# Kernel tuning notes

Measured on AMD Instinct MI355X. Metric: run time of the kernel, lower is better.

The kernel has to match this reference:

```python
import jax, jax.numpy as jnp
import numpy as np

N_GRAPHS = 128


def setup_inputs() -> dict:
    key = jax.random.key(0)
    k1, k2, k3, k4, k5, k6, k7 = jax.random.split(key, 7)
    N, E, IN, HID, OUT = 50000, 800000, 64, 64, 2
    x = jax.random.normal(k1, (N, IN), dtype=jnp.float32)
    edge_index = jax.random.randint(k2, (2, E), 0, N, dtype=jnp.int64)
    batch = jnp.sort(jax.random.randint(k3, (N,), 0, N_GRAPHS, dtype=jnp.int64))
    # GCNConv params (glorot-ish) and output Linear params
    W = jax.random.normal(k4, (IN, HID), dtype=jnp.float32) / np.sqrt(IN)
    b = jnp.zeros((HID,), dtype=jnp.float32)
    lin_W = jax.random.normal(k5, (HID, OUT), dtype=jnp.float32) / np.sqrt(HID)
    lin_b = jax.random.normal(k6, (OUT,), dtype=jnp.float32) * 0.01
    return {"x": x, "edge_index": edge_index, "batch": batch,
            "W": W, "b": b, "lin_W": lin_W, "lin_b": lin_b}


def gcn_conv(x, edge_index, W, b):
    N = x.shape[0]
    # add self loops (PyG GCNConv default)
    loop = jnp.arange(N, dtype=edge_index.dtype)
    row = jnp.concatenate([edge_index[0], loop])  # source nodes
    col = jnp.concatenate([edge_index[1], loop])  # target nodes
    # symmetric degree normalization D^{-1/2} (A+I) D^{-1/2}
    deg = jax.ops.segment_sum(jnp.ones_like(col, dtype=x.dtype), col, num_segments=N)
    dinv = jnp.where(deg > 0, jax.lax.rsqrt(jnp.maximum(deg, 1e-12)), 0.0)
    norm = dinv[row] * dinv[col]  # [E+N]
    h = x @ W  # [N, HID] transform before aggregation
    msgs = norm[:, None] * h[row]  # [E+N, HID] gathered messages
    out = jax.ops.segment_sum(msgs, col, num_segments=N)
    return out + b


def reference(x, edge_index, batch, W, b, lin_W, lin_b):
    h = gcn_conv(x, edge_index, W, b)
    h = jax.nn.relu(h)
    # global mean pool over batch ids
    sums = jax.ops.segment_sum(h, batch, num_segments=N_GRAPHS)  # [G, HID]
    cnts = jax.ops.segment_sum(jnp.ones((h.shape[0],), h.dtype), batch, num_segments=N_GRAPHS)
    pooled = sums / jnp.maximum(cnts, 1.0)[:, None]
    # dropout(p=0.2) is identity in eval mode
    return pooled @ lin_W + lin_b  # [G, OUT]
```

## Files before the change

kernel.cpp:

```cpp
#include <hip/hip_runtime.h>
#include <hip/hip_fp16.h>

#define N_NODES 50000
#define N_EDGES 800000
#define FDIM    64
#define NGRAPH  128
#define CAP     64
#define GW      8
#define NPB     32
#define NGSLOT  8
#define NBLK1   200
#define CHUNK_E (N_EDGES / NBLK1)
#define CHUNK_I4 (CHUNK_E / 4)
#define NBKT    196
#define SEGC    64


__global__ void k_bin(const int4* __restrict__ row4, const int4* __restrict__ col4,
                      unsigned int* __restrict__ gbin, int* __restrict__ gcnt,
                      float* __restrict__ pooled, float* __restrict__ cnt) {
    __shared__ unsigned int sbuf[NBKT * SEGC];
    __shared__ int scnt[NBKT];
    int tid = threadIdx.x, blk = blockIdx.x;
    if (blk == 0) {
        float4 z = make_float4(0.f, 0.f, 0.f, 0.f);
        float4* p4 = (float4*)pooled;
        for (int i = tid; i < (NGRAPH * FDIM) / 4; i += 256) p4[i] = z;
        float4* c4 = (float4*)cnt;
        if (tid < NGRAPH / 4) c4[tid] = z;
    }
    for (int i = tid; i < NBKT; i += 256) scnt[i] = 0;
    __syncthreads();
    int base = blk * CHUNK_I4;
    for (int i = base + tid; i < base + CHUNK_I4; i += 256) {
        int4 c = col4[i];
        int4 r = row4[i];
        int s, p;
        s = c.x >> 8; p = atomicAdd(&scnt[s], 1);
        if (p < SEGC) sbuf[s * SEGC + p] = ((unsigned)(c.x & 255) << 16) | (unsigned)r.x;
        s = c.y >> 8; p = atomicAdd(&scnt[s], 1);
        if (p < SEGC) sbuf[s * SEGC + p] = ((unsigned)(c.y & 255) << 16) | (unsigned)r.y;
        s = c.z >> 8; p = atomicAdd(&scnt[s], 1);
        if (p < SEGC) sbuf[s * SEGC + p] = ((unsigned)(c.z & 255) << 16) | (unsigned)r.z;
        s = c.w >> 8; p = atomicAdd(&scnt[s], 1);
        if (p < SEGC) sbuf[s * SEGC + p] = ((unsigned)(c.w & 255) << 16) | (unsigned)r.w;
    }
    __syncthreads();
    const uint4* s4 = (const uint4*)sbuf;
    uint4* g4 = (uint4*)(gbin + (size_t)blk * (NBKT * SEGC));
    for (int i = tid; i < NBKT * SEGC / 4; i += 256) g4[i] = s4[i];
    for (int s = tid; s < NBKT; s += 256) gcnt[s * NBLK1 + blk] = min(scnt[s], SEGC);
}

__global__ void k_commit(const unsigned int* __restrict__ gbin, const int* __restrict__ gcnt,
                         int* __restrict__ fill, unsigned short* __restrict__ ew) {
    __shared__ int cnts[NBLK1];
    __shared__ int fl[256];
    __shared__ unsigned short slots[256 * CAP];
    int b = blockIdx.x, tid = threadIdx.x;
    for (int i = tid; i < NBLK1; i += 256) cnts[i] = gcnt[b * NBLK1 + i];
    fl[tid] = 0;
    __syncthreads();
    for (int idx = tid; idx < NBLK1 * SEGC; idx += 256) {
        int seg = idx >> 6, j = idx & 63;
        if (j < cnts[seg]) {
            unsigned int v = gbin[((size_t)seg * NBKT + b) * SEGC + j];
            int cl = (int)(v >> 16);
            int p = atomicAdd(&fl[cl], 1);
            if (p < CAP) slots[(cl << 6) + p] = (unsigned short)(v & 0xffffu);
        }
    }
    __syncthreads();
    int nd0 = b << 8;
    int nnodes = min(256, N_NODES - nd0);
    uint4* e4 = (uint4*)(ew + ((size_t)nd0 << 6));
    const uint4* s4 = (const uint4*)slots;
    for (int i = tid; i < nnodes * 8; i += 256) e4[i] = s4[i];
    if (tid < nnodes) fill[nd0 + tid] = fl[tid];
}

__global__ void k_gemm_xw(const float* __restrict__ x, const float* __restrict__ W,
                          const int* __restrict__ fill, __half* __restrict__ h2, int n) {
    int f = threadIdx.x & 63;
    int w = threadIdx.x >> 6;
    float Wreg[FDIM];
    #pragma unroll
    for (int k = 0; k < FDIM; ++k) Wreg[k] = W[k * FDIM + f];
    for (int nd = blockIdx.x * 4 + w; nd < n; nd += gridDim.x * 4) {
        const float4* xr4 = (const float4*)(x + (size_t)nd * FDIM);
        float acc = 0.0f;
        #pragma unroll
        for (int k4 = 0; k4 < 16; ++k4) {
            float4 xv = xr4[k4];
            acc = fmaf(xv.x, Wreg[4 * k4],     acc);
            acc = fmaf(xv.y, Wreg[4 * k4 + 1], acc);
            acc = fmaf(xv.z, Wreg[4 * k4 + 2], acc);
            acc = fmaf(xv.w, Wreg[4 * k4 + 3], acc);
        }
        float di = rsqrtf((float)(fill[nd] + 1));
        h2[((size_t)nd << 6) + f] = __float2half(di * acc);
    }
}

#define ACC4(U, AX, AY, AZ, AW)                                        \
    {                                                                  \
        float2 lo_ = __half22float2(*(const __half2*)&(U).x);          \
        float2 hi_ = __half22float2(*(const __half2*)&(U).y);          \
        AX += lo_.x; AY += lo_.y; AZ += hi_.x; AW += hi_.y;            \
    }

__global__ void k_gather_pool(const int* __restrict__ fill, const unsigned short* __restrict__ ew,
                              const uint2* __restrict__ h2q, const float* __restrict__ b,
                              const int* __restrict__ batch,
                              float* __restrict__ pooled, float* __restrict__ cnt) {
    __shared__ float pl[NGSLOT][FDIM];
    __shared__ float pcnt[NGSLOT];
    __shared__ int g_first_s;

    int tid = threadIdx.x;
    int lane    = tid & 63;
    int fp      = lane & 15;
    int quarter = lane >> 4;
    int wv  = tid >> 6;
    int blk0 = blockIdx.x * NPB;

    for (int i = tid; i < NGSLOT * FDIM; i += 256) pl[i >> 6][i & 63] = 0.0f;
    if (tid < NGSLOT) pcnt[tid] = 0.0f;
    if (tid == 0) g_first_s = batch[blk0];
    __syncthreads();
    int g_first = g_first_s;

    int start = blk0 + wv * GW;
    bool active = start < N_NODES;

    if (active) {
        int dg8 = fill[start + (lane & 7)];
        int bt8 = batch[start + (lane & 7)];
        int slots = (int)ew[((size_t)start << 6) + lane];

        float b0 = b[4 * fp], b1 = b[4 * fp + 1], b2 = b[4 * fp + 2], b3 = b[4 * fp + 3];
        float p0 = 0, p1 = 0, p2 = 0, p3 = 0, cacc = 0;
        int gcur = __shfl(bt8, 0);
        #pragma unroll
        for (int i = 0; i < GW; ++i) {
            int nd = start + i;
            int slots_next = (i < GW - 1) ? (int)ew[((size_t)(nd + 1) << 6) + lane] : 0;
            int g = __shfl(bt8, i);
            if (g != gcur) {
                int sl = gcur - g_first;
                if (sl >= 0 && sl < NGSLOT) {
                    if (quarter == 0) {
                        atomicAdd(&pl[sl][4 * fp],     p0);
                        atomicAdd(&pl[sl][4 * fp + 1], p1);
                        atomicAdd(&pl[sl][4 * fp + 2], p2);
                        atomicAdd(&pl[sl][4 * fp + 3], p3);
                    }
                    if (lane == 0) atomicAdd(&pcnt[sl], cacc);
                } else {
                    if (quarter == 0) {
                        atomicAdd(&pooled[gcur * FDIM + 4 * fp],     p0);
                        atomicAdd(&pooled[gcur * FDIM + 4 * fp + 1], p1);
                        atomicAdd(&pooled[gcur * FDIM + 4 * fp + 2], p2);
                        atomicAdd(&pooled[gcur * FDIM + 4 * fp + 3], p3);
                    }
                    if (lane == 0) atomicAdd(&cnt[gcur], cacc);
                }
                p0 = p1 = p2 = p3 = 0; cacc = 0; gcur = g;
            }
            int deg = min(__shfl(dg8, i), CAP);
            float a0x = 0, a0y = 0, a0z = 0, a0w = 0;
            float a1x = 0, a1y = 0, a1z = 0, a1w = 0;
            float a2x = 0, a2y = 0, a2z = 0, a2w = 0;
            float a3x = 0, a3y = 0, a3z = 0, a3w = 0;
            if (quarter == 0) {
                uint2 su = h2q[((size_t)nd << 4) + fp];
                ACC4(su, a0x, a0y, a0z, a0w);
            }
            int e = 0;
            for (; e + 16 <= deg; e += 16) {
                int s0 = __shfl(slots, e + quarter);
                int s1 = __shfl(slots, e + 4 + quarter);
                int s2 = __shfl(slots, e + 8 + quarter);
                int s3 = __shfl(slots, e + 12 + quarter);
                uint2 u0 = h2q[((size_t)s0 << 4) + fp];
                uint2 u1 = h2q[((size_t)s1 << 4) + fp];
                uint2 u2 = h2q[((size_t)s2 << 4) + fp];
                uint2 u3 = h2q[((size_t)s3 << 4) + fp];
                ACC4(u0, a0x, a0y, a0z, a0w);
                ACC4(u1, a1x, a1y, a1z, a1w);
                ACC4(u2, a2x, a2y, a2z, a2w);
                ACC4(u3, a3x, a3y, a3z, a3w);
            }
            for (; e < deg; e += 4) {
                int idx = e + quarter;
                int sx = __shfl(slots, idx < deg ? idx : deg - 1);
                uint2 u = h2q[((size_t)sx << 4) + fp];
                if (idx < deg) ACC4(u, a0x, a0y, a0z, a0w);
            }
            float ax = (a0x + a1x) + (a2x + a3x);
            float ay = (a0y + a1y) + (a2y + a3y);
            float az = (a0z + a1z) + (a2z + a3z);
            float aw = (a0w + a1w) + (a2w + a3w);
            ax += __shfl_xor(ax, 16); ax += __shfl_xor(ax, 32);
            ay += __shfl_xor(ay, 16); ay += __shfl_xor(ay, 32);
            az += __shfl_xor(az, 16); az += __shfl_xor(az, 32);
            aw += __shfl_xor(aw, 16); aw += __shfl_xor(aw, 32);
            float di = rsqrtf((float)(deg + 1));
            p0 += fmaxf(fmaf(di, ax, b0), 0.0f);
            p1 += fmaxf(fmaf(di, ay, b1), 0.0f);
            p2 += fmaxf(fmaf(di, az, b2), 0.0f);
            p3 += fmaxf(fmaf(di, aw, b3), 0.0f);
            cacc += 1.0f;
            slots = slots_next;
        }
        {
            int sl = gcur - g_first;
            if (sl >= 0 && sl < NGSLOT) {
                if (quarter == 0) {
                    atomicAdd(&pl[sl][4 * fp],     p0);
                    atomicAdd(&pl[sl][4 * fp + 1], p1);
                    atomicAdd(&pl[sl][4 * fp + 2], p2);
                    atomicAdd(&pl[sl][4 * fp + 3], p3);
                }
                if (lane == 0) atomicAdd(&pcnt[sl], cacc);
            } else {
                if (quarter == 0) {
                    atomicAdd(&pooled[gcur * FDIM + 4 * fp],     p0);
                    atomicAdd(&pooled[gcur * FDIM + 4 * fp + 1], p1);
                    atomicAdd(&pooled[gcur * FDIM + 4 * fp + 2], p2);
                    atomicAdd(&pooled[gcur * FDIM + 4 * fp + 3], p3);
                }
                if (lane == 0) atomicAdd(&cnt[gcur], cacc);
            }
        }
    }
    __syncthreads();
    for (int idx = tid; idx < NGSLOT * FDIM; idx += 256) {
        int sl = idx >> 6, f = idx & 63;
        float v = pl[sl][f];
        if (v != 0.0f) atomicAdd(&pooled[(g_first + sl) * FDIM + f], v);
    }
    if (tid < NGSLOT) {
        float c = pcnt[tid];
        if (c != 0.0f) atomicAdd(&cnt[g_first + tid], c);
    }
}

__global__ void k_final_lin(const float* __restrict__ pooled, const float* __restrict__ cnt,
                            const float* __restrict__ linW, const float* __restrict__ linb,
                            float* __restrict__ out) {
    int t = threadIdx.x;
    int g = t >> 1;
    int o = t & 1;
    float c = fmaxf(cnt[g], 1.0f);
    float acc = 0.0f;
    #pragma unroll
    for (int k = 0; k < FDIM; ++k) acc = fmaf(pooled[g * FDIM + k], linW[k * 2 + o], acc);
    out[g * 2 + o] = acc / c + linb[o];
}


extern "C" void kernel_launch(void* const* d_in, const int* in_sizes, int n_in,
                              void* d_out, int out_size, void* d_ws, size_t ws_size,
                              hipStream_t stream) {
    const float* x      = (const float*)d_in[0];
    const int*   ei     = (const int*)d_in[1];
    const int*   batch  = (const int*)d_in[2];
    const float* W      = (const float*)d_in[3];
    const float* b      = (const float*)d_in[4];
    const float* linW   = (const float*)d_in[5];
    const float* linb   = (const float*)d_in[6];
    float*       out    = (float*)d_out;

    const int* row = ei;
    const int* col = ei + N_EDGES;

    char* ws = (char*)d_ws;
    size_t off = 0;
    float*          pooled = (float*)         (ws + off); off += (size_t)NGRAPH * FDIM * 4;
    float*          cnt    = (float*)         (ws + off); off += 512;
    int*            fill   = (int*)           (ws + off); off += ((size_t)N_NODES * 4 + 255) / 256 * 256;
    int*            gcnt   = (int*)           (ws + off); off += ((size_t)NBKT * NBLK1 * 4 + 255) / 256 * 256;
    unsigned int*   gbin   = (unsigned int*)  (ws + off); off += (size_t)NBLK1 * NBKT * SEGC * 4;
    unsigned short* ew     = (unsigned short*)(ws + off); off += (size_t)N_NODES * CAP * 2;
    __half*         h2     = (__half*)        (ws + off); off += (size_t)N_NODES * FDIM * 2;

    k_bin<<<NBLK1, 256, 0, stream>>>((const int4*)row, (const int4*)col, gbin, gcnt, pooled, cnt);

    k_commit<<<NBKT, 256, 0, stream>>>(gbin, gcnt, fill, ew);

    k_gemm_xw<<<1024, 256, 0, stream>>>(x, W, fill, h2, N_NODES);

    int nblocks = (N_NODES + NPB - 1) / NPB;
    k_gather_pool<<<nblocks, 256, 0, stream>>>(fill, ew, (const uint2*)h2, b, batch, pooled, cnt);

    k_final_lin<<<1, 256, 0, stream>>>(pooled, cnt, linW, linb, out);
}
```

Measured before the change: 91.31 us.

## Store transformed node features as fp8 and gather 8 features per lane

The intermediate h = D^-1/2 XW is now stored as fp8 instead of fp16, which halves the bytes touched by the random neighbor gathers. The gather kernel is reorganised so each lane decodes 8 fp8 features from a uint2, and 8 edges are processed per pass instead of 4. Edge-slot loads use nontemporal hints. The cost is a large loss of precision in the stored features, which may push the result past the accuracy tolerance, and more shuffle-reduction steps per node.

```diff
diff --git a/kernel.cpp b/kernel.cpp
--- a/kernel.cpp
+++ b/kernel.cpp
@@ -15,6 +15,8 @@
 #define NBKT    196
 #define SEGC    64
 
+using f32x2 = __attribute__((ext_vector_type(2))) float;
+
 
 __global__ void k_bin(const int4* __restrict__ row4, const int4* __restrict__ col4,
                       unsigned int* __restrict__ gbin, int* __restrict__ gcnt,
@@ -80,7 +82,7 @@
 }
 
 __global__ void k_gemm_xw(const float* __restrict__ x, const float* __restrict__ W,
-                          const int* __restrict__ fill, __half* __restrict__ h2, int n) {
+                          const int* __restrict__ fill, unsigned char* __restrict__ h2b, int n) {
     int f = threadIdx.x & 63;
     int w = threadIdx.x >> 6;
     float Wreg[FDIM];
@@ -98,15 +100,20 @@
             acc = fmaf(xv.w, Wreg[4 * k4 + 3], acc);
         }
         float di = rsqrtf((float)(fill[nd] + 1));
-        h2[((size_t)nd << 6) + f] = __float2half(di * acc);
-    }
-}
-
-#define ACC4(U, AX, AY, AZ, AW)                                        \
-    {                                                                  \
-        float2 lo_ = __half22float2(*(const __half2*)&(U).x);          \
-        float2 hi_ = __half22float2(*(const __half2*)&(U).y);          \
-        AX += lo_.x; AY += lo_.y; AZ += hi_.x; AW += hi_.y;            \
+        float v = di * acc;
+        int pk = __builtin_amdgcn_cvt_pk_fp8_f32(v, v, 0, false);
+        h2b[((size_t)nd << 6) + f] = (unsigned char)(pk & 0xff);
+    }
+}
+
+#define ACC8(U, A0, A1, A2, A3, A4, A5, A6, A7)                                   \
+    {                                                                             \
+        f32x2 p0_ = __builtin_amdgcn_cvt_pk_f32_fp8((int)(U).x, false);           \
+        f32x2 p1_ = __builtin_amdgcn_cvt_pk_f32_fp8((int)(U).x, true);            \
+        f32x2 p2_ = __builtin_amdgcn_cvt_pk_f32_fp8((int)(U).y, false);           \
+        f32x2 p3_ = __builtin_amdgcn_cvt_pk_f32_fp8((int)(U).y, true);            \
+        A0 += p0_.x; A1 += p0_.y; A2 += p1_.x; A3 += p1_.y;                       \
+        A4 += p2_.x; A5 += p2_.y; A6 += p3_.x; A7 += p3_.y;                       \
     }
 
 __global__ void k_gather_pool(const int* __restrict__ fill, const unsigned short* __restrict__ ew,
@@ -118,10 +125,10 @@
     __shared__ int g_first_s;
 
     int tid = threadIdx.x;
-    int lane    = tid & 63;
-    int fp      = lane & 15;
-    int quarter = lane >> 4;
-    int wv  = tid >> 6;
+    int lane = tid & 63;
+    int fp   = lane & 7;
+    int oct  = lane >> 3;
+    int wv   = tid >> 6;
     int blk0 = blockIdx.x * NPB;
 
     for (int i = tid; i < NGSLOT * FDIM; i += 256) pl[i >> 6][i & 63] = 0.0f;
@@ -136,99 +143,115 @@
     if (active) {
         int dg8 = fill[start + (lane & 7)];
         int bt8 = batch[start + (lane & 7)];
-        int slots = (int)ew[((size_t)start << 6) + lane];
-
-        float b0 = b[4 * fp], b1 = b[4 * fp + 1], b2 = b[4 * fp + 2], b3 = b[4 * fp + 3];
-        float p0 = 0, p1 = 0, p2 = 0, p3 = 0, cacc = 0;
+        int slots = (int)__builtin_nontemporal_load(&ew[((size_t)start << 6) + lane]);
+
+        float b0 = b[8 * fp],     b1 = b[8 * fp + 1], b2 = b[8 * fp + 2], b3 = b[8 * fp + 3];
+        float b4 = b[8 * fp + 4], b5 = b[8 * fp + 5], b6 = b[8 * fp + 6], b7 = b[8 * fp + 7];
+        float p0 = 0, p1 = 0, p2 = 0, p3 = 0, p4 = 0, p5 = 0, p6 = 0, p7 = 0, cacc = 0;
         int gcur = __shfl(bt8, 0);
         #pragma unroll
         for (int i = 0; i < GW; ++i) {
             int nd = start + i;
-            int slots_next = (i < GW - 1) ? (int)ew[((size_t)(nd + 1) << 6) + lane] : 0;
+            int slots_next = (i < GW - 1)
+                ? (int)__builtin_nontemporal_load(&ew[((size_t)(nd + 1) << 6) + lane]) : 0;
             int g = __shfl(bt8, i);
             if (g != gcur) {
                 int sl = gcur - g_first;
                 if (sl >= 0 && sl < NGSLOT) {
-                    if (quarter == 0) {
-                        atomicAdd(&pl[sl][4 * fp],     p0);
-                        atomicAdd(&pl[sl][4 * fp + 1], p1);
-                        atomicAdd(&pl[sl][4 * fp + 2], p2);
-                        atomicAdd(&pl[sl][4 * fp + 3], p3);
+                    if (oct == 0) {
+                        atomicAdd(&pl[sl][8 * fp],     p0);
+                        atomicAdd(&pl[sl][8 * fp + 1], p1);
+                        atomicAdd(&pl[sl][8 * fp + 2], p2);
+                        atomicAdd(&pl[sl][8 * fp + 3], p3);
+                        atomicAdd(&pl[sl][8 * fp + 4], p4);
+                        atomicAdd(&pl[sl][8 * fp + 5], p5);
+                        atomicAdd(&pl[sl][8 * fp + 6], p6);
+                        atomicAdd(&pl[sl][8 * fp + 7], p7);
                     }
                     if (lane == 0) atomicAdd(&pcnt[sl], cacc);
                 } else {
-                    if (quarter == 0) {
-                        atomicAdd(&pooled[gcur * FDIM + 4 * fp],     p0);
-                        atomicAdd(&pooled[gcur * FDIM + 4 * fp + 1], p1);
-                        atomicAdd(&pooled[gcur * FDIM + 4 * fp + 2], p2);
-                        atomicAdd(&pooled[gcur * FDIM + 4 * fp + 3], p3);
+                    if (oct == 0) {
+                        #pragma unroll
+                        for (int j = 0; j < 8; ++j) {
+                            float pv = j == 0 ? p0 : j == 1 ? p1 : j == 2 ? p2 : j == 3 ? p3
+                                     : j == 4 ? p4 : j == 5 ? p5 : j == 6 ? p6 : p7;
+                            atomicAdd(&pooled[gcur * FDIM + 8 * fp + j], pv);
+                        }
                     }
                     if (lane == 0) atomicAdd(&cnt[gcur], cacc);
                 }
-                p0 = p1 = p2 = p3 = 0; cacc = 0; gcur = g;
+                p0 = p1 = p2 = p3 = p4 = p5 = p6 = p7 = 0; cacc = 0; gcur = g;
             }
             int deg = min(__shfl(dg8, i), CAP);
-            float a0x = 0, a0y = 0, a0z = 0, a0w = 0;
-            float a1x = 0, a1y = 0, a1z = 0, a1w = 0;
-            float a2x = 0, a2y = 0, a2z = 0, a2w = 0;
-            float a3x = 0, a3y = 0, a3z = 0, a3w = 0;
-            if (quarter == 0) {
-                uint2 su = h2q[((size_t)nd << 4) + fp];
-                ACC4(su, a0x, a0y, a0z, a0w);
+            float a0 = 0, a1 = 0, a2 = 0, a3 = 0, a4 = 0, a5 = 0, a6 = 0, a7 = 0;
+            float c0 = 0, c1 = 0, c2 = 0, c3 = 0, c4 = 0, c5 = 0, c6 = 0, c7 = 0;
+            if (oct == 0) {
+                uint2 su = h2q[((size_t)nd << 3) + fp];
+                ACC8(su, a0, a1, a2, a3, a4, a5, a6, a7);
             }
             int e = 0;
             for (; e + 16 <= deg; e += 16) {
-                int s0 = __shfl(slots, e + quarter);
-                int s1 = __shfl(slots, e + 4 + quarter);
-                int s2 = __shfl(slots, e + 8 + quarter);
-                int s3 = __shfl(slots, e + 12 + quarter);
-                uint2 u0 = h2q[((size_t)s0 << 4) + fp];
-                uint2 u1 = h2q[((size_t)s1 << 4) + fp];
-                uint2 u2 = h2q[((size_t)s2 << 4) + fp];
-                uint2 u3 = h2q[((size_t)s3 << 4) + fp];
-                ACC4(u0, a0x, a0y, a0z, a0w);
-                ACC4(u1, a1x, a1y, a1z, a1w);
-                ACC4(u2, a2x, a2y, a2z, a2w);
-                ACC4(u3, a3x, a3y, a3z, a3w);
-            }
-            for (; e < deg; e += 4) {
-                int idx = e + quarter;
+                int s0 = __shfl(slots, e + oct);
+                int s1 = __shfl(slots, e + 8 + oct);
+                uint2 u0 = h2q[((size_t)s0 << 3) + fp];
+                uint2 u1 = h2q[((size_t)s1 << 3) + fp];
+                ACC8(u0, a0, a1, a2, a3, a4, a5, a6, a7);
+                ACC8(u1, c0, c1, c2, c3, c4, c5, c6, c7);
+            }
+            for (; e < deg; e += 8) {
+                int idx = e + oct;
                 int sx = __shfl(slots, idx < deg ? idx : deg - 1);
-                uint2 u = h2q[((size_t)sx << 4) + fp];
-                if (idx < deg) ACC4(u, a0x, a0y, a0z, a0w);
-            }
-            float ax = (a0x + a1x) + (a2x + a3x);
-            float ay = (a0y + a1y) + (a2y + a3y);
-            float az = (a0z + a1z) + (a2z + a3z);
-            float aw = (a0w + a1w) + (a2w + a3w);
-            ax += __shfl_xor(ax, 16); ax += __shfl_xor(ax, 32);
-            ay += __shfl_xor(ay, 16); ay += __shfl_xor(ay, 32);
-            az += __shfl_xor(az, 16); az += __shfl_xor(az, 32);
-            aw += __shfl_xor(aw, 16); aw += __shfl_xor(aw, 32);
+                uint2 u = h2q[((size_t)sx << 3) + fp];
+                if (idx < deg) ACC8(u, a0, a1, a2, a3, a4, a5, a6, a7);
+            }
+            a0 += c0; a1 += c1; a2 += c2; a3 += c3;
+            a4 += c4; a5 += c5; a6 += c6; a7 += c7;
+            a0 += __shfl_xor(a0, 8);  a1 += __shfl_xor(a1, 8);
+            a2 += __shfl_xor(a2, 8);  a3 += __shfl_xor(a3, 8);
+            a4 += __shfl_xor(a4, 8);  a5 += __shfl_xor(a5, 8);
+            a6 += __shfl_xor(a6, 8);  a7 += __shfl_xor(a7, 8);
+            a0 += __shfl_xor(a0, 16); a1 += __shfl_xor(a1, 16);
+            a2 += __shfl_xor(a2, 16); a3 += __shfl_xor(a3, 16);
+            a4 += __shfl_xor(a4, 16); a5 += __shfl_xor(a5, 16);
+            a6 += __shfl_xor(a6, 16); a7 += __shfl_xor(a7, 16);
+            a0 += __shfl_xor(a0, 32); a1 += __shfl_xor(a1, 32);
+            a2 += __shfl_xor(a2, 32); a3 += __shfl_xor(a3, 32);
+            a4 += __shfl_xor(a4, 32); a5 += __shfl_xor(a5, 32);
+            a6 += __shfl_xor(a6, 32); a7 += __shfl_xor(a7, 32);
             float di = rsqrtf((float)(deg + 1));
-            p0 += fmaxf(fmaf(di, ax, b0), 0.0f);
-            p1 += fmaxf(fmaf(di, ay, b1), 0.0f);
-            p2 += fmaxf(fmaf(di, az, b2), 0.0f);
-            p3 += fmaxf(fmaf(di, aw, b3), 0.0f);
+            p0 += fmaxf(fmaf(di, a0, b0), 0.0f);
+            p1 += fmaxf(fmaf(di, a1, b1), 0.0f);
+            p2 += fmaxf(fmaf(di, a2, b2), 0.0f);
+            p3 += fmaxf(fmaf(di, a3, b3), 0.0f);
+            p4 += fmaxf(fmaf(di, a4, b4), 0.0f);
+            p5 += fmaxf(fmaf(di, a5, b5), 0.0f);
+            p6 += fmaxf(fmaf(di, a6, b6), 0.0f);
+            p7 += fmaxf(fmaf(di, a7, b7), 0.0f);
             cacc += 1.0f;
             slots = slots_next;
         }
         {
             int sl = gcur - g_first;
             if (sl >= 0 && sl < NGSLOT) {
-                if (quarter == 0) {
-                    atomicAdd(&pl[sl][4 * fp],     p0);
-                    atomicAdd(&pl[sl][4 * fp + 1], p1);
-                    atomicAdd(&pl[sl][4 * fp + 2], p2);
-                    atomicAdd(&pl[sl][4 * fp + 3], p3);
+                if (oct == 0) {
+                    atomicAdd(&pl[sl][8 * fp],     p0);
+                    atomicAdd(&pl[sl][8 * fp + 1], p1);
+                    atomicAdd(&pl[sl][8 * fp + 2], p2);
+                    atomicAdd(&pl[sl][8 * fp + 3], p3);
+                    atomicAdd(&pl[sl][8 * fp + 4], p4);
+                    atomicAdd(&pl[sl][8 * fp + 5], p5);
+                    atomicAdd(&pl[sl][8 * fp + 6], p6);
+                    atomicAdd(&pl[sl][8 * fp + 7], p7);
                 }
                 if (lane == 0) atomicAdd(&pcnt[sl], cacc);
             } else {
-                if (quarter == 0) {
-                    atomicAdd(&pooled[gcur * FDIM + 4 * fp],     p0);
-                    atomicAdd(&pooled[gcur * FDIM + 4 * fp + 1], p1);
-                    atomicAdd(&pooled[gcur * FDIM + 4 * fp + 2], p2);
-                    atomicAdd(&pooled[gcur * FDIM + 4 * fp + 3], p3);
+                if (oct == 0) {
+                    #pragma unroll
+                    for (int j = 0; j < 8; ++j) {
+                        float pv = j == 0 ? p0 : j == 1 ? p1 : j == 2 ? p2 : j == 3 ? p3
+                                 : j == 4 ? p4 : j == 5 ? p5 : j == 6 ? p6 : p7;
+                        atomicAdd(&pooled[gcur * FDIM + 8 * fp + j], pv);
+                    }
                 }
                 if (lane == 0) atomicAdd(&cnt[gcur], cacc);
             }
@@ -283,7 +306,7 @@
     int*            gcnt   = (int*)           (ws + off); off += ((size_t)NBKT * NBLK1 * 4 + 255) / 256 * 256;
     unsigned int*   gbin   = (unsigned int*)  (ws + off); off += (size_t)NBLK1 * NBKT * SEGC * 4;
     unsigned short* ew     = (unsigned short*)(ws + off); off += (size_t)N_NODES * CAP * 2;
-    __half*         h2     = (__half*)        (ws + off); off += (size_t)N_NODES * FDIM * 2;
+    unsigned char*  h2     = (unsigned char*) (ws + off); off += (size_t)N_NODES * FDIM;
 
     k_bin<<<NBLK1, 256, 0, stream>>>((const int4*)row, (const int4*)col, gbin, gcnt, pooled, cnt);
 
```

After: 92.99 us. About the same (+1.8%).
